# Performance work log

Measured on AMD Instinct MI355X. Metric: run time of the kernel, lower is better.

The kernel has to match this reference:

```python
import jax, jax.numpy as jnp
import numpy as np

N = 100000   # nodes
E = 1600000  # directed edges (avg degree 16)
IN, HID, OUT = 32, 64, 32


def setup_inputs() -> dict:
    key = jax.random.key(0)
    k0, k1, k2, k3 = jax.random.split(key, 4)
    x = jax.random.normal(k0, (N, IN), dtype=jnp.float32)
    edge_index = jax.random.randint(k1, (2, E), 0, N, dtype=jnp.int32)
    W1 = jax.random.normal(k2, (IN, HID), dtype=jnp.float32) * (1.0 / np.sqrt(IN))
    b1 = jnp.zeros((HID,), dtype=jnp.float32)
    W2 = jax.random.normal(k3, (HID, OUT), dtype=jnp.float32) * (1.0 / np.sqrt(HID))
    b2 = jnp.zeros((OUT,), dtype=jnp.float32)
    return {"x": x, "edge_index": edge_index, "W1": W1, "b1": b1, "W2": W2, "b2": b2}


def gcn_conv(x, src, dst, W, b, n):
    # GCNConv: D^{-1/2} (A + I) D^{-1/2} X W + b, deg computed after self-loops
    h = x @ W                                   # [N, d_out]
    ones = jnp.ones_like(dst, dtype=h.dtype)
    deg = jax.ops.segment_sum(ones, dst, num_segments=n)   # >= 1 (self-loops)
    dinv = jax.lax.rsqrt(jnp.maximum(deg, 1.0))
    norm = dinv[src] * dinv[dst]                # [E + N]
    agg = jax.ops.segment_sum(norm[:, None] * h[src], dst, num_segments=n)
    return agg + b


def reference(x, edge_index, W1, b1, W2, b2):
    n = x.shape[0]
    loop = jnp.arange(n, dtype=edge_index.dtype)
    src = jnp.concatenate([edge_index[0], loop])  # add self-loops once
    dst = jnp.concatenate([edge_index[1], loop])
    h = jax.nn.relu(gcn_conv(x, src, dst, W1, b1, n))
    # dropout omitted (eval mode)
    out = gcn_conv(h, src, dst, W2, b2, n)
    return out
```

## Files before the change

kernel.cpp:

```cpp
#include <hip/hip_runtime.h>

#define IN_F  32
#define HID_F 64
#define OUT_F 32

#define BKT_SHIFT 8
#define BKT_NODES 256
#define NBLK      512

__device__ inline unsigned short f2bf(float f) {
    unsigned u = __float_as_uint(f);
    return (unsigned short)((u + 0x7FFF + ((u >> 16) & 1)) >> 16);
}
__device__ inline float bflo(unsigned w) { return __uint_as_float(w << 16); }
__device__ inline float bfhi(unsigned w) { return __uint_as_float(w & 0xFFFF0000u); }

__global__ __launch_bounds__(256) void count_kernel(const int* __restrict__ dst,
                                                    int* __restrict__ cnt, int E, int nb)
{
    __shared__ int hist[1024];
    int tid = threadIdx.x;
    for (int i = tid; i < nb; i += 256) hist[i] = 0;
    __syncthreads();
    for (int e = blockIdx.x * 256 + tid; e < E; e += NBLK * 256)
        atomicAdd(&hist[dst[e] >> BKT_SHIFT], 1);
    __syncthreads();
    for (int i = tid; i < nb; i += 256) cnt[i * NBLK + blockIdx.x] = hist[i];
}

__global__ __launch_bounds__(NBLK) void bsum_kernel(const int* __restrict__ cnt,
                                                    int* __restrict__ bsum)
{
    __shared__ int s[NBLK];
    int tid = threadIdx.x, b = blockIdx.x;
    s[tid] = cnt[b * NBLK + tid];
    __syncthreads();
    for (int off = NBLK / 2; off > 0; off >>= 1) {
        if (tid < off) s[tid] += s[tid + off];
        __syncthreads();
    }
    if (tid == 0) bsum[b] = s[0];
}

__global__ __launch_bounds__(512) void bscan_kernel(int* __restrict__ bsum, int nb,
                                                    int* __restrict__ cellstart, int nc,
                                                    int* __restrict__ rowstart, int n, int E)
{
    __shared__ int s[512];
    int tid = threadIdx.x;
    int my = (tid < nb) ? bsum[tid] : 0;
    s[tid] = my;
    __syncthreads();
    for (int off = 1; off < 512; off <<= 1) {
        int t = (tid >= off) ? s[tid - off] : 0;
        __syncthreads();
        s[tid] += t;
        __syncthreads();
    }
    if (tid < nb) bsum[tid] = s[tid] - my;
    if (tid == 0) { cellstart[nc] = E; rowstart[n] = E; }
}

__global__ __launch_bounds__(NBLK) void cscan_kernel(const int* __restrict__ cnt,
                                                     const int* __restrict__ bsum,
                                                     int* __restrict__ cellstart)
{
    __shared__ int s[NBLK];
    int tid = threadIdx.x, b = blockIdx.x;
    int my = cnt[b * NBLK + tid];
    s[tid] = my;
    __syncthreads();
    for (int off = 1; off < NBLK; off <<= 1) {
        int t = (tid >= off) ? s[tid - off] : 0;
        __syncthreads();
        s[tid] += t;
        __syncthreads();
    }
    cellstart[b * NBLK + tid] = bsum[b] + s[tid] - my;
}

__global__ __launch_bounds__(256) void append_kernel(
    const int* __restrict__ src, const int* __restrict__ dst,
    const int* __restrict__ cellstart, unsigned* __restrict__ pairs, int E, int nb)
{
    __shared__ int cur[1024];
    int tid = threadIdx.x;
    for (int i = tid; i < nb; i += 256) cur[i] = cellstart[i * NBLK + blockIdx.x];
    __syncthreads();
    for (int e = blockIdx.x * 256 + tid; e < E; e += NBLK * 256) {
        int d = dst[e];
        int pos = atomicAdd(&cur[d >> BKT_SHIFT], 1);
        pairs[pos] = ((unsigned)src[e] << BKT_SHIFT) | (unsigned)(d & (BKT_NODES - 1));
    }
}

__global__ __launch_bounds__(256) void place_kernel(
    const int* __restrict__ cellstart, const unsigned* __restrict__ pairs,
    int* __restrict__ srcs, int* __restrict__ rowstart, float* __restrict__ dinv, int n)
{
    __shared__ int hist[BKT_NODES];
    __shared__ int ofs[BKT_NODES];
    int b = blockIdx.x, tid = threadIdx.x;
    int beg = cellstart[b * NBLK], end = cellstart[(b + 1) * NBLK];
    hist[tid] = 0;
    __syncthreads();
    for (int e = beg + tid; e < end; e += 256)
        atomicAdd(&hist[pairs[e] & (BKT_NODES - 1)], 1);
    __syncthreads();
    int my = hist[tid];
    ofs[tid] = my;
    __syncthreads();
    for (int off = 1; off < 256; off <<= 1) {
        int t = (tid >= off) ? ofs[tid - off] : 0;
        __syncthreads();
        ofs[tid] += t;
        __syncthreads();
    }
    int excl = ofs[tid] - my;
    int node = b * BKT_NODES + tid;
    if (node < n) {
        rowstart[node] = beg + excl;
        dinv[node] = rsqrtf((float)(my + 1));
    }
    __syncthreads();
    ofs[tid] = excl;
    __syncthreads();
    for (int e = beg + tid; e < end; e += 256) {
        unsigned p = pairs[e];
        int dl = p & (BKT_NODES - 1);
        int pos = beg + atomicAdd(&ofs[dl], 1);
        srcs[pos] = (int)(p >> BKT_SHIFT);
    }
}

__global__ void xs_kernel(const float* __restrict__ x, const float* __restrict__ dinv,
                          unsigned short* __restrict__ xsb, int n) {
    int t = blockIdx.x * blockDim.x + threadIdx.x;
    if (t < n * (IN_F / 4)) {
        float d = dinv[t >> 3];
        float4 v = ((const float4*)x)[t];
        ushort4 o;
        o.x = f2bf(v.x * d); o.y = f2bf(v.y * d);
        o.z = f2bf(v.z * d); o.w = f2bf(v.w * d);
        ((ushort4*)xsb)[t] = o;
    }
}

__global__ __launch_bounds__(256) void fused1_kernel(
    const int* __restrict__ rowstart, const int* __restrict__ srcs,
    const unsigned* __restrict__ xs2, const float* __restrict__ dinv,
    const float* __restrict__ b1, const float* __restrict__ W1,
    const float* __restrict__ W2, unsigned* __restrict__ hs2p, int n)
{
    __shared__ float W1s[IN_F * HID_F];
    __shared__ float W2s[HID_F * OUT_F];
    __shared__ float grow[16][IN_F + 1];
    __shared__ float hrow[16][HID_F + 1];
    int tid = threadIdx.x;
    for (int t = tid; t < IN_F * HID_F; t += 256) W1s[t] = W1[t];
    for (int t = tid; t < HID_F * OUT_F; t += 256) W2s[t] = W2[t];

    int nl = tid >> 4;
    unsigned q = tid & 15;
    int node = blockIdx.x * 16 + nl;
    bool active = node < n;
    int nodec = active ? node : 0;

    int beg = rowstart[nodec], end = active ? rowstart[nodec + 1] : beg;
    unsigned ws = active ? xs2[((unsigned)nodec << 4) + q] : 0u;
    float a0l = bflo(ws), a0h = bfhi(ws);
    float a1l = 0.f, a1h = 0.f, a2l = 0.f, a2h = 0.f, a3l = 0.f, a3h = 0.f;
    float a4l = 0.f, a4h = 0.f, a5l = 0.f, a5h = 0.f, a6l = 0.f, a6h = 0.f;
    float a7l = 0.f, a7h = 0.f;
    int e = beg;
    for (; e + 8 <= end; e += 8) {
        unsigned o0 = ((unsigned)srcs[e]     << 4) + q, o1 = ((unsigned)srcs[e + 1] << 4) + q;
        unsigned o2 = ((unsigned)srcs[e + 2] << 4) + q, o3 = ((unsigned)srcs[e + 3] << 4) + q;
        unsigned o4 = ((unsigned)srcs[e + 4] << 4) + q, o5 = ((unsigned)srcs[e + 5] << 4) + q;
        unsigned o6 = ((unsigned)srcs[e + 6] << 4) + q, o7 = ((unsigned)srcs[e + 7] << 4) + q;
        unsigned w0 = xs2[o0], w1 = xs2[o1], w2 = xs2[o2], w3 = xs2[o3];
        unsigned w4 = xs2[o4], w5 = xs2[o5], w6 = xs2[o6], w7 = xs2[o7];
        a0l += bflo(w0); a0h += bfhi(w0); a1l += bflo(w1); a1h += bfhi(w1);
        a2l += bflo(w2); a2h += bfhi(w2); a3l += bflo(w3); a3h += bfhi(w3);
        a4l += bflo(w4); a4h += bfhi(w4); a5l += bflo(w5); a5h += bfhi(w5);
        a6l += bflo(w6); a6h += bfhi(w6); a7l += bflo(w7); a7h += bfhi(w7);
    }
    for (; e + 4 <= end; e += 4) {
        unsigned o0 = ((unsigned)srcs[e]     << 4) + q, o1 = ((unsigned)srcs[e + 1] << 4) + q;
        unsigned o2 = ((unsigned)srcs[e + 2] << 4) + q, o3 = ((unsigned)srcs[e + 3] << 4) + q;
        unsigned w0 = xs2[o0], w1 = xs2[o1], w2 = xs2[o2], w3 = xs2[o3];
        a0l += bflo(w0); a0h += bfhi(w0); a1l += bflo(w1); a1h += bfhi(w1);
        a2l += bflo(w2); a2h += bfhi(w2); a3l += bflo(w3); a3h += bfhi(w3);
    }
    for (; e < end; ++e) {
        unsigned w0 = xs2[((unsigned)srcs[e] << 4) + q];
        a0l += bflo(w0); a0h += bfhi(w0);
    }
    float dv = dinv[nodec];
    grow[nl][2 * q]     = dv * (((a0l + a1l) + (a2l + a3l)) + ((a4l + a5l) + (a6l + a7l)));
    grow[nl][2 * q + 1] = dv * (((a0h + a1h) + (a2h + a3h)) + ((a4h + a5h) + (a6h + a7h)));
    __syncthreads();

    float h0 = b1[q], h1 = b1[q + 16], h2 = b1[q + 32], h3 = b1[q + 48];
    #pragma unroll
    for (int k = 0; k < IN_F; ++k) {
        float gk = grow[nl][k];
        h0 += gk * W1s[k * HID_F + q];
        h1 += gk * W1s[k * HID_F + q + 16];
        h2 += gk * W1s[k * HID_F + q + 32];
        h3 += gk * W1s[k * HID_F + q + 48];
    }
    hrow[nl][q]      = fmaxf(h0, 0.f);
    hrow[nl][q + 16] = fmaxf(h1, 0.f);
    hrow[nl][q + 32] = fmaxf(h2, 0.f);
    hrow[nl][q + 48] = fmaxf(h3, 0.f);
    __syncthreads();

    float p0 = 0.f, p1 = 0.f;
    #pragma unroll
    for (int k = 0; k < HID_F; ++k) {
        float hk = hrow[nl][k];
        p0 += hk * W2s[k * OUT_F + 2 * q];
        p1 += hk * W2s[k * OUT_F + 2 * q + 1];
    }
    if (active) {
        unsigned pack = (unsigned)f2bf(dv * p0) | ((unsigned)f2bf(dv * p1) << 16);
        hs2p[((unsigned)node << 4) + q] = pack;
    }
}

__global__ __launch_bounds__(256) void agg2_kernel(
    const int* __restrict__ rowstart, const int* __restrict__ srcs,
    const unsigned* __restrict__ hs2p, const float* __restrict__ dinv,
    const float* __restrict__ b2, float* __restrict__ out, int n)
{
    int t = blockIdx.x * blockDim.x + threadIdx.x;
    int node = t >> 4;
    if (node >= n) return;
    unsigned q = t & 15;
    int beg = rowstart[node], end = rowstart[node + 1];
    unsigned ws = hs2p[((unsigned)node << 4) + q];
    float a0l = bflo(ws), a0h = bfhi(ws);
    float a1l = 0.f, a1h = 0.f, a2l = 0.f, a2h = 0.f, a3l = 0.f, a3h = 0.f;
    float a4l = 0.f, a4h = 0.f, a5l = 0.f, a5h = 0.f, a6l = 0.f, a6h = 0.f;
    float a7l = 0.f, a7h = 0.f;
    int e = beg;
    for (; e + 8 <= end; e += 8) {
        unsigned o0 = ((unsigned)srcs[e]     << 4) + q, o1 = ((unsigned)srcs[e + 1] << 4) + q;
        unsigned o2 = ((unsigned)srcs[e + 2] << 4) + q, o3 = ((unsigned)srcs[e + 3] << 4) + q;
        unsigned o4 = ((unsigned)srcs[e + 4] << 4) + q, o5 = ((unsigned)srcs[e + 5] << 4) + q;
        unsigned o6 = ((unsigned)srcs[e + 6] << 4) + q, o7 = ((unsigned)srcs[e + 7] << 4) + q;
        unsigned w0 = hs2p[o0], w1 = hs2p[o1], w2 = hs2p[o2], w3 = hs2p[o3];
        unsigned w4 = hs2p[o4], w5 = hs2p[o5], w6 = hs2p[o6], w7 = hs2p[o7];
        a0l += bflo(w0); a0h += bfhi(w0); a1l += bflo(w1); a1h += bfhi(w1);
        a2l += bflo(w2); a2h += bfhi(w2); a3l += bflo(w3); a3h += bfhi(w3);
        a4l += bflo(w4); a4h += bfhi(w4); a5l += bflo(w5); a5h += bfhi(w5);
        a6l += bflo(w6); a6h += bfhi(w6); a7l += bflo(w7); a7h += bfhi(w7);
    }
    for (; e + 4 <= end; e += 4) {
        unsigned o0 = ((unsigned)srcs[e]     << 4) + q, o1 = ((unsigned)srcs[e + 1] << 4) + q;
        unsigned o2 = ((unsigned)srcs[e + 2] << 4) + q, o3 = ((unsigned)srcs[e + 3] << 4) + q;
        unsigned w0 = hs2p[o0], w1 = hs2p[o1], w2 = hs2p[o2], w3 = hs2p[o3];
        a0l += bflo(w0); a0h += bfhi(w0); a1l += bflo(w1); a1h += bfhi(w1);
        a2l += bflo(w2); a2h += bfhi(w2); a3l += bflo(w3); a3h += bfhi(w3);
    }
    for (; e < end; ++e) {
        unsigned w0 = hs2p[((unsigned)srcs[e] << 4) + q];
        a0l += bflo(w0); a0h += bfhi(w0);
    }
    float dvv = dinv[node];
    float2 r;
    r.x = dvv * (((a0l + a1l) + (a2l + a3l)) + ((a4l + a5l) + (a6l + a7l))) + b2[2 * q];
    r.y = dvv * (((a0h + a1h) + (a2h + a3h)) + ((a4h + a5h) + (a6h + a7h))) + b2[2 * q + 1];
    ((float2*)out)[((size_t)node << 4) + q] = r;
}

extern "C" void kernel_launch(void* const* d_in, const int* in_sizes, int n_in,
                              void* d_out, int out_size, void* d_ws, size_t ws_size,
                              hipStream_t stream) {
    const float* x  = (const float*)d_in[0];
    const int*   ei = (const int*)  d_in[1];
    const float* W1 = (const float*)d_in[2];
    const float* b1 = (const float*)d_in[3];
    const float* W2 = (const float*)d_in[4];
    const float* b2 = (const float*)d_in[5];
    float* out = (float*)d_out;

    const int n = in_sizes[0] / IN_F;
    const int E = in_sizes[1] / 2;
    const int* src = ei;
    const int* dst = ei + E;

    const int nb = (n + BKT_NODES - 1) >> BKT_SHIFT;
    const int nc = nb * NBLK;

    int* ip = (int*)d_ws;
    int* cnt       = ip;                 ip += nc;
    int* cellstart = ip;                 ip += nc + 1;
    int* bsum      = ip;                 ip += nb + 1;
    int* rowstart  = ip;                 ip += n + 1;
    unsigned* pairs = (unsigned*)ip;     ip += E;
    int* srcs_srt  = ip;                 ip += E;
    float* dinv = (float*)ip;            ip += n;
    unsigned* xs2  = (unsigned*)ip;      ip += (size_t)n * IN_F / 2;
    unsigned* hs2p = (unsigned*)ip;

    count_kernel<<<NBLK, 256, 0, stream>>>(dst, cnt, E, nb);
    bsum_kernel <<<nb, NBLK, 0, stream>>>(cnt, bsum);
    bscan_kernel<<<1, 512, 0, stream>>>(bsum, nb, cellstart, nc, rowstart, n, E);
    cscan_kernel<<<nb, NBLK, 0, stream>>>(cnt, bsum, cellstart);
    append_kernel<<<NBLK, 256, 0, stream>>>(src, dst, cellstart, pairs, E, nb);
    place_kernel<<<nb, 256, 0, stream>>>(cellstart, pairs, srcs_srt, rowstart, dinv, n);

    xs_kernel<<<((size_t)n * 8 + 255) / 256, 256, 0, stream>>>(x, dinv, (unsigned short*)xs2, n);

    fused1_kernel<<<(n + 15) / 16, 256, 0, stream>>>(rowstart, srcs_srt, xs2, dinv, b1, W1, W2, hs2p, n);
    agg2_kernel<<<((size_t)n * 16 + 255) / 256, 256, 0, stream>>>(rowstart, srcs_srt, hs2p, dinv, b2, out, n);
}
```

Measured before the change: 215.5 us.

## Split edge gathers by source-node half to shrink the random-access working set

Edges are bucketed by whether the source lies in the lower or upper half of the node range, which gives two CSR row-start arrays. Each aggregation then runs as two passes, one per source half. The first pass writes float2 partial sums to a buffer and the second adds them in. The aim is to keep each pass's random gather table (about half of 3.2 MB of bf16 features) resident in cache. The cost is two extra kernel launches, extra partial-sum traffic of n×32 floats per layer, a larger scan, and a separate dinv kernel.

Result: slower. 237.0 us (+10.0%).

```diff
diff --git a/kernel.cpp b/kernel.cpp
--- a/kernel.cpp
+++ b/kernel.cpp
@@ -15,15 +15,20 @@
 __device__ inline float bflo(unsigned w) { return __uint_as_float(w << 16); }
 __device__ inline float bfhi(unsigned w) { return __uint_as_float(w & 0xFFFF0000u); }
 
-__global__ __launch_bounds__(256) void count_kernel(const int* __restrict__ dst,
-                                                    int* __restrict__ cnt, int E, int nb)
+__global__ __launch_bounds__(256) void count_kernel(const int* __restrict__ src,
+                                                    const int* __restrict__ dst,
+                                                    int* __restrict__ cnt, int E,
+                                                    int nb0, int half_n)
 {
     __shared__ int hist[1024];
     int tid = threadIdx.x;
+    int nb = 2 * nb0;
     for (int i = tid; i < nb; i += 256) hist[i] = 0;
     __syncthreads();
-    for (int e = blockIdx.x * 256 + tid; e < E; e += NBLK * 256)
-        atomicAdd(&hist[dst[e] >> BKT_SHIFT], 1);
+    for (int e = blockIdx.x * 256 + tid; e < E; e += NBLK * 256) {
+        int cell = ((src[e] >= half_n) ? nb0 : 0) + (dst[e] >> BKT_SHIFT);
+        atomicAdd(&hist[cell], 1);
+    }
     __syncthreads();
     for (int i = tid; i < nb; i += 256) cnt[i * NBLK + blockIdx.x] = hist[i];
 }
@@ -42,23 +47,22 @@
     if (tid == 0) bsum[b] = s[0];
 }
 
-__global__ __launch_bounds__(512) void bscan_kernel(int* __restrict__ bsum, int nb,
-                                                    int* __restrict__ cellstart, int nc,
-                                                    int* __restrict__ rowstart, int n, int E)
-{
-    __shared__ int s[512];
+__global__ __launch_bounds__(1024) void bscan_kernel(int* __restrict__ bsum, int nb,
+                                                     int* __restrict__ cellstart, int nc, int E)
+{
+    __shared__ int s[1024];
     int tid = threadIdx.x;
     int my = (tid < nb) ? bsum[tid] : 0;
     s[tid] = my;
     __syncthreads();
-    for (int off = 1; off < 512; off <<= 1) {
+    for (int off = 1; off < 1024; off <<= 1) {
         int t = (tid >= off) ? s[tid - off] : 0;
         __syncthreads();
         s[tid] += t;
         __syncthreads();
     }
     if (tid < nb) bsum[tid] = s[tid] - my;
-    if (tid == 0) { cellstart[nc] = E; rowstart[n] = E; }
+    if (tid == 0) cellstart[nc] = E;
 }
 
 __global__ __launch_bounds__(NBLK) void cscan_kernel(const int* __restrict__ cnt,
@@ -81,27 +85,34 @@
 
 __global__ __launch_bounds__(256) void append_kernel(
     const int* __restrict__ src, const int* __restrict__ dst,
-    const int* __restrict__ cellstart, unsigned* __restrict__ pairs, int E, int nb)
+    const int* __restrict__ cellstart, unsigned* __restrict__ pairs, int E,
+    int nb0, int half_n)
 {
     __shared__ int cur[1024];
     int tid = threadIdx.x;
+    int nb = 2 * nb0;
     for (int i = tid; i < nb; i += 256) cur[i] = cellstart[i * NBLK + blockIdx.x];
     __syncthreads();
     for (int e = blockIdx.x * 256 + tid; e < E; e += NBLK * 256) {
-        int d = dst[e];
-        int pos = atomicAdd(&cur[d >> BKT_SHIFT], 1);
-        pairs[pos] = ((unsigned)src[e] << BKT_SHIFT) | (unsigned)(d & (BKT_NODES - 1));
+        int s = src[e], d = dst[e];
+        int cell = ((s >= half_n) ? nb0 : 0) + (d >> BKT_SHIFT);
+        int pos = atomicAdd(&cur[cell], 1);
+        pairs[pos] = ((unsigned)s << BKT_SHIFT) | (unsigned)(d & (BKT_NODES - 1));
     }
 }
 
 __global__ __launch_bounds__(256) void place_kernel(
     const int* __restrict__ cellstart, const unsigned* __restrict__ pairs,
-    int* __restrict__ srcs, int* __restrict__ rowstart, float* __restrict__ dinv, int n)
+    int* __restrict__ srcs, int* __restrict__ rs_lo, int* __restrict__ rs_hi,
+    int n, int nb0)
 {
     __shared__ int hist[BKT_NODES];
     __shared__ int ofs[BKT_NODES];
-    int b = blockIdx.x, tid = threadIdx.x;
-    int beg = cellstart[b * NBLK], end = cellstart[(b + 1) * NBLK];
+    int c = blockIdx.x, tid = threadIdx.x;
+    int half = (c >= nb0) ? 1 : 0;
+    int b = c - half * nb0;
+    int* rs = half ? rs_hi : rs_lo;
+    int beg = cellstart[c * NBLK], end = cellstart[(c + 1) * NBLK];
     hist[tid] = 0;
     __syncthreads();
     for (int e = beg + tid; e < end; e += 256)
@@ -118,10 +129,8 @@
     }
     int excl = ofs[tid] - my;
     int node = b * BKT_NODES + tid;
-    if (node < n) {
-        rowstart[node] = beg + excl;
-        dinv[node] = rsqrtf((float)(my + 1));
-    }
+    if (node < n)  rs[node] = beg + excl;
+    if (node == n - 1) rs[n] = beg + excl + my;
     __syncthreads();
     ofs[tid] = excl;
     __syncthreads();
@@ -130,6 +139,16 @@
         int dl = p & (BKT_NODES - 1);
         int pos = beg + atomicAdd(&ofs[dl], 1);
         srcs[pos] = (int)(p >> BKT_SHIFT);
+    }
+}
+
+__global__ void dinv_kernel(const int* __restrict__ rs_lo, const int* __restrict__ rs_hi,
+                            float* __restrict__ dinv, int n)
+{
+    int i = blockIdx.x * blockDim.x + threadIdx.x;
+    if (i < n) {
+        int deg = (rs_lo[i + 1] - rs_lo[i]) + (rs_hi[i + 1] - rs_hi[i]);
+        dinv[i] = rsqrtf((float)(deg + 1));
     }
 }
 
@@ -146,11 +165,55 @@
     }
 }
 
-__global__ __launch_bounds__(256) void fused1_kernel(
-    const int* __restrict__ rowstart, const int* __restrict__ srcs,
-    const unsigned* __restrict__ xs2, const float* __restrict__ dinv,
-    const float* __restrict__ b1, const float* __restrict__ W1,
-    const float* __restrict__ W2, unsigned* __restrict__ hs2p, int n)
+__global__ __launch_bounds__(256) void gather_half_kernel(
+    const int* __restrict__ rs, const int* __restrict__ srcs,
+    const unsigned* __restrict__ tab, float2* __restrict__ acc, int n)
+{
+    int tid = threadIdx.x;
+    int nl = tid >> 4;
+    unsigned q = tid & 15;
+    int node = blockIdx.x * 16 + nl;
+    if (node >= n) return;
+    int beg = rs[node], end = rs[node + 1];
+    float a0l = 0.f, a0h = 0.f, a1l = 0.f, a1h = 0.f, a2l = 0.f, a2h = 0.f;
+    float a3l = 0.f, a3h = 0.f, a4l = 0.f, a4h = 0.f, a5l = 0.f, a5h = 0.f;
+    float a6l = 0.f, a6h = 0.f, a7l = 0.f, a7h = 0.f;
+    int e = beg;
+    for (; e + 8 <= end; e += 8) {
+        unsigned o0 = ((unsigned)srcs[e]     << 4) + q, o1 = ((unsigned)srcs[e + 1] << 4) + q;
+        unsigned o2 = ((unsigned)srcs[e + 2] << 4) + q, o3 = ((unsigned)srcs[e + 3] << 4) + q;
+        unsigned o4 = ((unsigned)srcs[e + 4] << 4) + q, o5 = ((unsigned)srcs[e + 5] << 4) + q;
+        unsigned o6 = ((unsigned)srcs[e + 6] << 4) + q, o7 = ((unsigned)srcs[e + 7] << 4) + q;
+        unsigned w0 = tab[o0], w1 = tab[o1], w2 = tab[o2], w3 = tab[o3];
+        unsigned w4 = tab[o4], w5 = tab[o5], w6 = tab[o6], w7 = tab[o7];
+        a0l += bflo(w0); a0h += bfhi(w0); a1l += bflo(w1); a1h += bfhi(w1);
+        a2l += bflo(w2); a2h += bfhi(w2); a3l += bflo(w3); a3h += bfhi(w3);
+        a4l += bflo(w4); a4h += bfhi(w4); a5l += bflo(w5); a5h += bfhi(w5);
+        a6l += bflo(w6); a6h += bfhi(w6); a7l += bflo(w7); a7h += bfhi(w7);
+    }
+    for (; e + 4 <= end; e += 4) {
+        unsigned o0 = ((unsigned)srcs[e]     << 4) + q, o1 = ((unsigned)srcs[e + 1] << 4) + q;
+        unsigned o2 = ((unsigned)srcs[e + 2] << 4) + q, o3 = ((unsigned)srcs[e + 3] << 4) + q;
+        unsigned w0 = tab[o0], w1 = tab[o1], w2 = tab[o2], w3 = tab[o3];
+        a0l += bflo(w0); a0h += bfhi(w0); a1l += bflo(w1); a1h += bfhi(w1);
+        a2l += bflo(w2); a2h += bfhi(w2); a3l += bflo(w3); a3h += bfhi(w3);
+    }
+    for (; e < end; ++e) {
+        unsigned w0 = tab[((unsigned)srcs[e] << 4) + q];
+        a0l += bflo(w0); a0h += bfhi(w0);
+    }
+    float2 r;
+    r.x = ((a0l + a1l) + (a2l + a3l)) + ((a4l + a5l) + (a6l + a7l));
+    r.y = ((a0h + a1h) + (a2h + a3h)) + ((a4h + a5h) + (a6h + a7h));
+    acc[((unsigned)node << 4) + q] = r;
+}
+
+__global__ __launch_bounds__(256) void fused1b_kernel(
+    const int* __restrict__ rs_hi, const int* __restrict__ srcs,
+    const unsigned* __restrict__ xs2, const float2* __restrict__ acc,
+    const float* __restrict__ dinv, const float* __restrict__ b1,
+    const float* __restrict__ W1, const float* __restrict__ W2,
+    unsigned* __restrict__ hs2p, int n)
 {
     __shared__ float W1s[IN_F * HID_F];
     __shared__ float W2s[HID_F * OUT_F];
@@ -166,12 +229,10 @@
     bool active = node < n;
     int nodec = active ? node : 0;
 
-    int beg = rowstart[nodec], end = active ? rowstart[nodec + 1] : beg;
-    unsigned ws = active ? xs2[((unsigned)nodec << 4) + q] : 0u;
-    float a0l = bflo(ws), a0h = bfhi(ws);
-    float a1l = 0.f, a1h = 0.f, a2l = 0.f, a2h = 0.f, a3l = 0.f, a3h = 0.f;
-    float a4l = 0.f, a4h = 0.f, a5l = 0.f, a5h = 0.f, a6l = 0.f, a6h = 0.f;
-    float a7l = 0.f, a7h = 0.f;
+    int beg = rs_hi[nodec], end = active ? rs_hi[nodec + 1] : beg;
+    float a0l = 0.f, a0h = 0.f, a1l = 0.f, a1h = 0.f, a2l = 0.f, a2h = 0.f;
+    float a3l = 0.f, a3h = 0.f, a4l = 0.f, a4h = 0.f, a5l = 0.f, a5h = 0.f;
+    float a6l = 0.f, a6h = 0.f, a7l = 0.f, a7h = 0.f;
     int e = beg;
     for (; e + 8 <= end; e += 8) {
         unsigned o0 = ((unsigned)srcs[e]     << 4) + q, o1 = ((unsigned)srcs[e + 1] << 4) + q;
@@ -196,9 +257,15 @@
         unsigned w0 = xs2[((unsigned)srcs[e] << 4) + q];
         a0l += bflo(w0); a0h += bfhi(w0);
     }
+    float suml = ((a0l + a1l) + (a2l + a3l)) + ((a4l + a5l) + (a6l + a7l));
+    float sumh = ((a0h + a1h) + (a2h + a3h)) + ((a4h + a5h) + (a6h + a7h));
+    float2 a = acc[((unsigned)nodec << 4) + q];
+    unsigned ws = xs2[((unsigned)nodec << 4) + q];
+    suml += a.x + bflo(ws);
+    sumh += a.y + bfhi(ws);
     float dv = dinv[nodec];
-    grow[nl][2 * q]     = dv * (((a0l + a1l) + (a2l + a3l)) + ((a4l + a5l) + (a6l + a7l)));
-    grow[nl][2 * q + 1] = dv * (((a0h + a1h) + (a2h + a3h)) + ((a4h + a5h) + (a6h + a7h)));
+    grow[nl][2 * q]     = dv * suml;
+    grow[nl][2 * q + 1] = dv * sumh;
     __syncthreads();
 
     float h0 = b1[q], h1 = b1[q + 16], h2 = b1[q + 32], h3 = b1[q + 48];
@@ -229,21 +296,21 @@
     }
 }
 
-__global__ __launch_bounds__(256) void agg2_kernel(
-    const int* __restrict__ rowstart, const int* __restrict__ srcs,
-    const unsigned* __restrict__ hs2p, const float* __restrict__ dinv,
-    const float* __restrict__ b2, float* __restrict__ out, int n)
-{
-    int t = blockIdx.x * blockDim.x + threadIdx.x;
-    int node = t >> 4;
+__global__ __launch_bounds__(256) void agg2hi_kernel(
+    const int* __restrict__ rs_hi, const int* __restrict__ srcs,
+    const unsigned* __restrict__ hs2p, const float2* __restrict__ acc,
+    const float* __restrict__ dinv, const float* __restrict__ b2,
+    float* __restrict__ out, int n)
+{
+    int tid = threadIdx.x;
+    int nl = tid >> 4;
+    unsigned q = tid & 15;
+    int node = blockIdx.x * 16 + nl;
     if (node >= n) return;
-    unsigned q = t & 15;
-    int beg = rowstart[node], end = rowstart[node + 1];
-    unsigned ws = hs2p[((unsigned)node << 4) + q];
-    float a0l = bflo(ws), a0h = bfhi(ws);
-    float a1l = 0.f, a1h = 0.f, a2l = 0.f, a2h = 0.f, a3l = 0.f, a3h = 0.f;
-    float a4l = 0.f, a4h = 0.f, a5l = 0.f, a5h = 0.f, a6l = 0.f, a6h = 0.f;
-    float a7l = 0.f, a7h = 0.f;
+    int beg = rs_hi[node], end = rs_hi[node + 1];
+    float a0l = 0.f, a0h = 0.f, a1l = 0.f, a1h = 0.f, a2l = 0.f, a2h = 0.f;
+    float a3l = 0.f, a3h = 0.f, a4l = 0.f, a4h = 0.f, a5l = 0.f, a5h = 0.f;
+    float a6l = 0.f, a6h = 0.f, a7l = 0.f, a7h = 0.f;
     int e = beg;
     for (; e + 8 <= end; e += 8) {
         unsigned o0 = ((unsigned)srcs[e]     << 4) + q, o1 = ((unsigned)srcs[e + 1] << 4) + q;
@@ -268,10 +335,14 @@
         unsigned w0 = hs2p[((unsigned)srcs[e] << 4) + q];
         a0l += bflo(w0); a0h += bfhi(w0);
     }
+    float2 a = acc[((unsigned)node << 4) + q];
+    unsigned ws = hs2p[((unsigned)node << 4) + q];
+    float suml = ((a0l + a1l) + (a2l + a3l)) + ((a4l + a5l) + (a6l + a7l)) + a.x + bflo(ws);
+    float sumh = ((a0h + a1h) + (a2h + a3h)) + ((a4h + a5h) + (a6h + a7h)) + a.y + bfhi(ws);
     float dvv = dinv[node];
     float2 r;
-    r.x = dvv * (((a0l + a1l) + (a2l + a3l)) + ((a4l + a5l) + (a6l + a7l))) + b2[2 * q];
-    r.y = dvv * (((a0h + a1h) + (a2h + a3h)) + ((a4h + a5h) + (a6h + a7h))) + b2[2 * q + 1];
+    r.x = dvv * suml + b2[2 * q];
+    r.y = dvv * sumh + b2[2 * q + 1];
     ((float2*)out)[((size_t)node << 4) + q] = r;
 }
 
@@ -291,29 +362,36 @@
     const int* src = ei;
     const int* dst = ei + E;
 
-    const int nb = (n + BKT_NODES - 1) >> BKT_SHIFT;
-    const int nc = nb * NBLK;
+    const int half_n = n >> 1;
+    const int nb0 = (n + BKT_NODES - 1) >> BKT_SHIFT;
+    const int nb  = 2 * nb0;
+    const int nc  = nb * NBLK;
 
     int* ip = (int*)d_ws;
     int* cnt       = ip;                 ip += nc;
     int* cellstart = ip;                 ip += nc + 1;
     int* bsum      = ip;                 ip += nb + 1;
-    int* rowstart  = ip;                 ip += n + 1;
+    int* rs_lo     = ip;                 ip += n + 1;
+    int* rs_hi     = ip;                 ip += n + 1;
     unsigned* pairs = (unsigned*)ip;     ip += E;
     int* srcs_srt  = ip;                 ip += E;
     float* dinv = (float*)ip;            ip += n;
     unsigned* xs2  = (unsigned*)ip;      ip += (size_t)n * IN_F / 2;
-    unsigned* hs2p = (unsigned*)ip;
-
-    count_kernel<<<NBLK, 256, 0, stream>>>(dst, cnt, E, nb);
+    unsigned* hs2p = (unsigned*)ip;      ip += (size_t)n * IN_F / 2;
+    float2* acc    = (float2*)ip;
+
+    count_kernel<<<NBLK, 256, 0, stream>>>(src, dst, cnt, E, nb0, half_n);
     bsum_kernel <<<nb, NBLK, 0, stream>>>(cnt, bsum);
-    bscan_kernel<<<1, 512, 0, stream>>>(bsum, nb, cellstart, nc, rowstart, n, E);
+    bscan_kernel<<<1, 1024, 0, stream>>>(bsum, nb, cellstart, nc, E);
     cscan_kernel<<<nb, NBLK, 0, stream>>>(cnt, bsum, cellstart);
-    append_kernel<<<NBLK, 256, 0, stream>>>(src, dst, cellstart, pairs, E, nb);
-    place_kernel<<<nb, 256, 0, stream>>>(cellstart, pairs, srcs_srt, rowstart, dinv, n);
-
+    append_kernel<<<NBLK, 256, 0, stream>>>(src, dst, cellstart, pairs, E, nb0, half_n);
+    place_kernel<<<nb, 256, 0, stream>>>(cellstart, pairs, srcs_srt, rs_lo, rs_hi, n, nb0);
+    dinv_kernel<<<(n + 255) / 256, 256, 0, stream>>>(rs_lo, rs_hi, dinv, n);
     xs_kernel<<<((size_t)n * 8 + 255) / 256, 256, 0, stream>>>(x, dinv, (unsigned short*)xs2, n);
 
-    fused1_kernel<<<(n + 15) / 16, 256, 0, stream>>>(rowstart, srcs_srt, xs2, dinv, b1, W1, W2, hs2p, n);
-    agg2_kernel<<<((size_t)n * 16 + 255) / 256, 256, 0, stream>>>(rowstart, srcs_srt, hs2p, dinv, b2, out, n);
-}
+    const int ngrid = (n + 15) / 16;
+    gather_half_kernel<<<ngrid, 256, 0, stream>>>(rs_lo, srcs_srt, xs2, acc, n);
+    fused1b_kernel<<<ngrid, 256, 0, stream>>>(rs_hi, srcs_srt, xs2, acc, dinv, b1, W1, W2, hs2p, n);
+    gather_half_kernel<<<ngrid, 256, 0, stream>>>(rs_lo, srcs_srt, hs2p, acc, n);
+    agg2hi_kernel<<<ngrid, 256, 0, stream>>>(rs_hi, srcs_srt, hs2p, acc, dinv, b2, out, n);
+}
```

## Fuse bf16 feature scaling into place kernel and widen gathers to 8-byte loads

Applied to the files above, without the earlier changes.

Folds the separate xs_kernel into place_kernel. Each bucket block scales its nodes' features by dinv, kept in shared memory, and writes the packed bf16 table, which removes one launch and one dinv read pass. Both aggregation kernels now have each lane load 8 bytes (four bf16 values) per neighbour, with the two half-groups of 8 lanes working on alternating edges and combined by a shuffle. This halves the number of gather instructions per row. In fused1, the weights are pre-transposed into padded shared layouts for float4/float2 reads, and the intra-kernel barriers are dropped because each node's 16 lanes sit in one wavefront. The risk is relying on wavefront-local LDS ordering in place of the removed barriers, plus some idle lanes in the odd-edge tail and the final output write.

Result: slower. 229.7 us (+6.6%).

```diff
diff --git a/kernel.cpp b/kernel.cpp
--- a/kernel.cpp
+++ b/kernel.cpp
@@ -96,10 +96,13 @@
 
 __global__ __launch_bounds__(256) void place_kernel(
     const int* __restrict__ cellstart, const unsigned* __restrict__ pairs,
-    int* __restrict__ srcs, int* __restrict__ rowstart, float* __restrict__ dinv, int n)
+    const float* __restrict__ x,
+    int* __restrict__ srcs, int* __restrict__ rowstart, float* __restrict__ dinv,
+    unsigned* __restrict__ xs2, int n)
 {
     __shared__ int hist[BKT_NODES];
     __shared__ int ofs[BKT_NODES];
+    __shared__ float sdinv[BKT_NODES];
     int b = blockIdx.x, tid = threadIdx.x;
     int beg = cellstart[b * NBLK], end = cellstart[(b + 1) * NBLK];
     hist[tid] = 0;
@@ -118,9 +121,11 @@
     }
     int excl = ofs[tid] - my;
     int node = b * BKT_NODES + tid;
+    float dv = rsqrtf((float)(my + 1));
+    sdinv[tid] = dv;
     if (node < n) {
         rowstart[node] = beg + excl;
-        dinv[node] = rsqrtf((float)(my + 1));
+        dinv[node] = dv;
     }
     __syncthreads();
     ofs[tid] = excl;
@@ -131,18 +136,18 @@
         int pos = beg + atomicAdd(&ofs[dl], 1);
         srcs[pos] = (int)(p >> BKT_SHIFT);
     }
-}
-
-__global__ void xs_kernel(const float* __restrict__ x, const float* __restrict__ dinv,
-                          unsigned short* __restrict__ xsb, int n) {
-    int t = blockIdx.x * blockDim.x + threadIdx.x;
-    if (t < n * (IN_F / 4)) {
-        float d = dinv[t >> 3];
-        float4 v = ((const float4*)x)[t];
-        ushort4 o;
-        o.x = f2bf(v.x * d); o.y = f2bf(v.y * d);
-        o.z = f2bf(v.z * d); o.w = f2bf(v.w * d);
-        ((ushort4*)xsb)[t] = o;
+    const float4* x4 = (const float4*)x;
+    uint2* xo = (uint2*)xs2;
+    for (int idx = tid; idx < BKT_NODES * 8; idx += 256) {
+        int nloc = idx >> 3, g = idx & 7;
+        int nd = b * BKT_NODES + nloc;
+        if (nd < n) {
+            float d = sdinv[nloc];
+            float4 v = x4[((size_t)nd << 3) + g];
+            unsigned lo = (unsigned)f2bf(v.x * d) | ((unsigned)f2bf(v.y * d) << 16);
+            unsigned hi = (unsigned)f2bf(v.z * d) | ((unsigned)f2bf(v.w * d) << 16);
+            xo[((size_t)nd << 3) + g] = make_uint2(lo, hi);
+        }
     }
 }
 
@@ -152,76 +157,93 @@
     const float* __restrict__ b1, const float* __restrict__ W1,
     const float* __restrict__ W2, unsigned* __restrict__ hs2p, int n)
 {
-    __shared__ float W1s[IN_F * HID_F];
-    __shared__ float W2s[HID_F * OUT_F];
-    __shared__ float grow[16][IN_F + 1];
-    __shared__ float hrow[16][HID_F + 1];
-    int tid = threadIdx.x;
-    for (int t = tid; t < IN_F * HID_F; t += 256) W1s[t] = W1[t];
-    for (int t = tid; t < HID_F * OUT_F; t += 256) W2s[t] = W2[t];
+    __shared__ float W1ps[16 * 132];
+    __shared__ float W2ps[16 * 132];
+    __shared__ float grow[16 * 48];
+    __shared__ float hrow[16 * 80];
+    int tid = threadIdx.x;
+    for (int t = tid; t < 16 * 32; t += 256) {
+        int q = t >> 5, k = t & 31;
+        *(float4*)&W1ps[q * 132 + k * 4] =
+            make_float4(W1[k * HID_F + q],      W1[k * HID_F + q + 16],
+                        W1[k * HID_F + q + 32], W1[k * HID_F + q + 48]);
+    }
+    const float2* W2f2 = (const float2*)W2;
+    for (int t = tid; t < 16 * 64; t += 256) {
+        int q = t >> 6, k = t & 63;
+        *(float2*)&W2ps[q * 132 + k * 2] = W2f2[k * 16 + q];
+    }
+    __syncthreads();
 
     int nl = tid >> 4;
-    unsigned q = tid & 15;
+    int p  = tid & 15;
+    unsigned r = p & 7;
+    int hp = p >> 3;
     int node = blockIdx.x * 16 + nl;
     bool active = node < n;
     int nodec = active ? node : 0;
-
     int beg = rowstart[nodec], end = active ? rowstart[nodec + 1] : beg;
-    unsigned ws = active ? xs2[((unsigned)nodec << 4) + q] : 0u;
-    float a0l = bflo(ws), a0h = bfhi(ws);
-    float a1l = 0.f, a1h = 0.f, a2l = 0.f, a2h = 0.f, a3l = 0.f, a3h = 0.f;
-    float a4l = 0.f, a4h = 0.f, a5l = 0.f, a5h = 0.f, a6l = 0.f, a6h = 0.f;
-    float a7l = 0.f, a7h = 0.f;
+
+    const uint2* tab = (const uint2*)xs2;
+    float a00=0,a01=0,a02=0,a03=0, a10=0,a11=0,a12=0,a13=0;
+    float a20=0,a21=0,a22=0,a23=0, a30=0,a31=0,a32=0,a33=0;
     int e = beg;
     for (; e + 8 <= end; e += 8) {
-        unsigned o0 = ((unsigned)srcs[e]     << 4) + q, o1 = ((unsigned)srcs[e + 1] << 4) + q;
-        unsigned o2 = ((unsigned)srcs[e + 2] << 4) + q, o3 = ((unsigned)srcs[e + 3] << 4) + q;
-        unsigned o4 = ((unsigned)srcs[e + 4] << 4) + q, o5 = ((unsigned)srcs[e + 5] << 4) + q;
-        unsigned o6 = ((unsigned)srcs[e + 6] << 4) + q, o7 = ((unsigned)srcs[e + 7] << 4) + q;
-        unsigned w0 = xs2[o0], w1 = xs2[o1], w2 = xs2[o2], w3 = xs2[o3];
-        unsigned w4 = xs2[o4], w5 = xs2[o5], w6 = xs2[o6], w7 = xs2[o7];
-        a0l += bflo(w0); a0h += bfhi(w0); a1l += bflo(w1); a1h += bfhi(w1);
-        a2l += bflo(w2); a2h += bfhi(w2); a3l += bflo(w3); a3h += bfhi(w3);
-        a4l += bflo(w4); a4h += bfhi(w4); a5l += bflo(w5); a5h += bfhi(w5);
-        a6l += bflo(w6); a6h += bfhi(w6); a7l += bflo(w7); a7h += bfhi(w7);
-    }
-    for (; e + 4 <= end; e += 4) {
-        unsigned o0 = ((unsigned)srcs[e]     << 4) + q, o1 = ((unsigned)srcs[e + 1] << 4) + q;
-        unsigned o2 = ((unsigned)srcs[e + 2] << 4) + q, o3 = ((unsigned)srcs[e + 3] << 4) + q;
-        unsigned w0 = xs2[o0], w1 = xs2[o1], w2 = xs2[o2], w3 = xs2[o3];
-        a0l += bflo(w0); a0h += bfhi(w0); a1l += bflo(w1); a1h += bfhi(w1);
-        a2l += bflo(w2); a2h += bfhi(w2); a3l += bflo(w3); a3h += bfhi(w3);
-    }
-    for (; e < end; ++e) {
-        unsigned w0 = xs2[((unsigned)srcs[e] << 4) + q];
-        a0l += bflo(w0); a0h += bfhi(w0);
-    }
+        int i0 = srcs[e + 0 + hp], i1 = srcs[e + 2 + hp];
+        int i2 = srcs[e + 4 + hp], i3 = srcs[e + 6 + hp];
+        uint2 w0 = tab[((unsigned)i0 << 3) + r];
+        uint2 w1 = tab[((unsigned)i1 << 3) + r];
+        uint2 w2 = tab[((unsigned)i2 << 3) + r];
+        uint2 w3 = tab[((unsigned)i3 << 3) + r];
+        a00 += bflo(w0.x); a01 += bfhi(w0.x); a02 += bflo(w0.y); a03 += bfhi(w0.y);
+        a10 += bflo(w1.x); a11 += bfhi(w1.x); a12 += bflo(w1.y); a13 += bfhi(w1.y);
+        a20 += bflo(w2.x); a21 += bfhi(w2.x); a22 += bflo(w2.y); a23 += bfhi(w2.y);
+        a30 += bflo(w3.x); a31 += bfhi(w3.x); a32 += bflo(w3.y); a33 += bfhi(w3.y);
+    }
+    for (; e + 2 <= end; e += 2) {
+        int i0 = srcs[e + hp];
+        uint2 w0 = tab[((unsigned)i0 << 3) + r];
+        a00 += bflo(w0.x); a01 += bfhi(w0.x); a02 += bflo(w0.y); a03 += bfhi(w0.y);
+    }
+    if (e < end && hp == 0) {
+        int i0 = srcs[e];
+        uint2 w0 = tab[((unsigned)i0 << 3) + r];
+        a00 += bflo(w0.x); a01 += bfhi(w0.x); a02 += bflo(w0.y); a03 += bfhi(w0.y);
+    }
+    if (hp == 0) {
+        uint2 w0 = tab[((unsigned)nodec << 3) + r];
+        a10 += bflo(w0.x); a11 += bfhi(w0.x); a12 += bflo(w0.y); a13 += bfhi(w0.y);
+    }
+    float f0 = (a00 + a10) + (a20 + a30);
+    float f1 = (a01 + a11) + (a21 + a31);
+    float f2 = (a02 + a12) + (a22 + a32);
+    float f3 = (a03 + a13) + (a23 + a33);
+    f0 += __shfl_xor(f0, 8); f1 += __shfl_xor(f1, 8);
+    f2 += __shfl_xor(f2, 8); f3 += __shfl_xor(f3, 8);
     float dv = dinv[nodec];
-    grow[nl][2 * q]     = dv * (((a0l + a1l) + (a2l + a3l)) + ((a4l + a5l) + (a6l + a7l)));
-    grow[nl][2 * q + 1] = dv * (((a0h + a1h) + (a2h + a3h)) + ((a4h + a5h) + (a6h + a7h)));
-    __syncthreads();
-
+    if (hp == 0)
+        *(float4*)&grow[nl * 48 + (int)r * 4] = make_float4(dv*f0, dv*f1, dv*f2, dv*f3);
+
+    int q = p;
     float h0 = b1[q], h1 = b1[q + 16], h2 = b1[q + 32], h3 = b1[q + 48];
+    const float4* w1r = (const float4*)&W1ps[q * 132];
     #pragma unroll
     for (int k = 0; k < IN_F; ++k) {
-        float gk = grow[nl][k];
-        h0 += gk * W1s[k * HID_F + q];
-        h1 += gk * W1s[k * HID_F + q + 16];
-        h2 += gk * W1s[k * HID_F + q + 32];
-        h3 += gk * W1s[k * HID_F + q + 48];
-    }
-    hrow[nl][q]      = fmaxf(h0, 0.f);
-    hrow[nl][q + 16] = fmaxf(h1, 0.f);
-    hrow[nl][q + 32] = fmaxf(h2, 0.f);
-    hrow[nl][q + 48] = fmaxf(h3, 0.f);
-    __syncthreads();
-
+        float gk = grow[nl * 48 + k];
+        float4 w = w1r[k];
+        h0 += gk * w.x; h1 += gk * w.y; h2 += gk * w.z; h3 += gk * w.w;
+    }
+    hrow[nl * 80 + q]      = fmaxf(h0, 0.f);
+    hrow[nl * 80 + q + 16] = fmaxf(h1, 0.f);
+    hrow[nl * 80 + q + 32] = fmaxf(h2, 0.f);
+    hrow[nl * 80 + q + 48] = fmaxf(h3, 0.f);
     float p0 = 0.f, p1 = 0.f;
+    const float2* w2r = (const float2*)&W2ps[q * 132];
     #pragma unroll
     for (int k = 0; k < HID_F; ++k) {
-        float hk = hrow[nl][k];
-        p0 += hk * W2s[k * OUT_F + 2 * q];
-        p1 += hk * W2s[k * OUT_F + 2 * q + 1];
+        float hk = hrow[nl * 80 + k];
+        float2 w = w2r[k];
+        p0 += hk * w.x; p1 += hk * w.y;
     }
     if (active) {
         unsigned pack = (unsigned)f2bf(dv * p0) | ((unsigned)f2bf(dv * p1) << 16);
@@ -234,45 +256,57 @@
     const unsigned* __restrict__ hs2p, const float* __restrict__ dinv,
     const float* __restrict__ b2, float* __restrict__ out, int n)
 {
-    int t = blockIdx.x * blockDim.x + threadIdx.x;
-    int node = t >> 4;
+    int tid = threadIdx.x;
+    int nl = tid >> 4, p = tid & 15;
+    unsigned r = p & 7;
+    int hp = p >> 3;
+    int node = blockIdx.x * 16 + nl;
     if (node >= n) return;
-    unsigned q = t & 15;
     int beg = rowstart[node], end = rowstart[node + 1];
-    unsigned ws = hs2p[((unsigned)node << 4) + q];
-    float a0l = bflo(ws), a0h = bfhi(ws);
-    float a1l = 0.f, a1h = 0.f, a2l = 0.f, a2h = 0.f, a3l = 0.f, a3h = 0.f;
-    float a4l = 0.f, a4h = 0.f, a5l = 0.f, a5h = 0.f, a6l = 0.f, a6h = 0.f;
-    float a7l = 0.f, a7h = 0.f;
+    const uint2* tab = (const uint2*)hs2p;
+    float a00=0,a01=0,a02=0,a03=0, a10=0,a11=0,a12=0,a13=0;
+    float a20=0,a21=0,a22=0,a23=0, a30=0,a31=0,a32=0,a33=0;
     int e = beg;
     for (; e + 8 <= end; e += 8) {
-        unsigned o0 = ((unsigned)srcs[e]     << 4) + q, o1 = ((unsigned)srcs[e + 1] << 4) + q;
-        unsigned o2 = ((unsigned)srcs[e + 2] << 4) + q, o3 = ((unsigned)srcs[e + 3] << 4) + q;
-        unsigned o4 = ((unsigned)srcs[e + 4] << 4) + q, o5 = ((unsigned)srcs[e + 5] << 4) + q;
-        unsigned o6 = ((unsigned)srcs[e + 6] << 4) + q, o7 = ((unsigned)srcs[e + 7] << 4) + q;
-        unsigned w0 = hs2p[o0], w1 = hs2p[o1], w2 = hs2p[o2], w3 = hs2p[o3];
-        unsigned w4 = hs2p[o4], w5 = hs2p[o5], w6 = hs2p[o6], w7 = hs2p[o7];
-        a0l += bflo(w0); a0h += bfhi(w0); a1l += bflo(w1); a1h += bfhi(w1);
-        a2l += bflo(w2); a2h += bfhi(w2); a3l += bflo(w3); a3h += bfhi(w3);
-        a4l += bflo(w4); a4h += bfhi(w4); a5l += bflo(w5); a5h += bfhi(w5);
-        a6l += bflo(w6); a6h += bfhi(w6); a7l += bflo(w7); a7h += bfhi(w7);
-    }
-    for (; e + 4 <= end; e += 4) {
-        unsigned o0 = ((unsigned)srcs[e]     << 4) + q, o1 = ((unsigned)srcs[e + 1] << 4) + q;
-        unsigned o2 = ((unsigned)srcs[e + 2] << 4) + q, o3 = ((unsigned)srcs[e + 3] << 4) + q;
-        unsigned w0 = hs2p[o0], w1 = hs2p[o1], w2 = hs2p[o2], w3 = hs2p[o3];
-        a0l += bflo(w0); a0h += bfhi(w0); a1l += bflo(w1); a1h += bfhi(w1);
-        a2l += bflo(w2); a2h += bfhi(w2); a3l += bflo(w3); a3h += bfhi(w3);
-    }
-    for (; e < end; ++e) {
-        unsigned w0 = hs2p[((unsigned)srcs[e] << 4) + q];
-        a0l += bflo(w0); a0h += bfhi(w0);
-    }
-    float dvv = dinv[node];
-    float2 r;
-    r.x = dvv * (((a0l + a1l) + (a2l + a3l)) + ((a4l + a5l) + (a6l + a7l))) + b2[2 * q];
-    r.y = dvv * (((a0h + a1h) + (a2h + a3h)) + ((a4h + a5h) + (a6h + a7h))) + b2[2 * q + 1];
-    ((float2*)out)[((size_t)node << 4) + q] = r;
+        int i0 = srcs[e + 0 + hp], i1 = srcs[e + 2 + hp];
+        int i2 = srcs[e + 4 + hp], i3 = srcs[e + 6 + hp];
+        uint2 w0 = tab[((unsigned)i0 << 3) + r];
+        uint2 w1 = tab[((unsigned)i1 << 3) + r];
+        uint2 w2 = tab[((unsigned)i2 << 3) + r];
+        uint2 w3 = tab[((unsigned)i3 << 3) + r];
+        a00 += bflo(w0.x); a01 += bfhi(w0.x); a02 += bflo(w0.y); a03 += bfhi(w0.y);
+        a10 += bflo(w1.x); a11 += bfhi(w1.x); a12 += bflo(w1.y); a13 += bfhi(w1.y);
+        a20 += bflo(w2.x); a21 += bfhi(w2.x); a22 += bflo(w2.y); a23 += bfhi(w2.y);
+        a30 += bflo(w3.x); a31 += bfhi(w3.x); a32 += bflo(w3.y); a33 += bfhi(w3.y);
+    }
+    for (; e + 2 <= end; e += 2) {
+        int i0 = srcs[e + hp];
+        uint2 w0 = tab[((unsigned)i0 << 3) + r];
+        a00 += bflo(w0.x); a01 += bfhi(w0.x); a02 += bflo(w0.y); a03 += bfhi(w0.y);
+    }
+    if (e < end && hp == 0) {
+        int i0 = srcs[e];
+        uint2 w0 = tab[((unsigned)i0 << 3) + r];
+        a00 += bflo(w0.x); a01 += bfhi(w0.x); a02 += bflo(w0.y); a03 += bfhi(w0.y);
+    }
+    if (hp == 0) {
+        uint2 w0 = tab[((unsigned)node << 3) + r];
+        a10 += bflo(w0.x); a11 += bfhi(w0.x); a12 += bflo(w0.y); a13 += bfhi(w0.y);
+    }
+    float f0 = (a00 + a10) + (a20 + a30);
+    float f1 = (a01 + a11) + (a21 + a31);
+    float f2 = (a02 + a12) + (a22 + a32);
+    float f3 = (a03 + a13) + (a23 + a33);
+    f0 += __shfl_xor(f0, 8); f1 += __shfl_xor(f1, 8);
+    f2 += __shfl_xor(f2, 8); f3 += __shfl_xor(f3, 8);
+    if (hp == 0) {
+        float dvv = dinv[node];
+        float4 bb = ((const float4*)b2)[r];
+        float4 o;
+        o.x = dvv * f0 + bb.x; o.y = dvv * f1 + bb.y;
+        o.z = dvv * f2 + bb.z; o.w = dvv * f3 + bb.w;
+        ((float4*)out)[((size_t)node << 3) + r] = o;
+    }
 }
 
 extern "C" void kernel_launch(void* const* d_in, const int* in_sizes, int n_in,
@@ -310,10 +344,9 @@
     bscan_kernel<<<1, 512, 0, stream>>>(bsum, nb, cellstart, nc, rowstart, n, E);
     cscan_kernel<<<nb, NBLK, 0, stream>>>(cnt, bsum, cellstart);
     append_kernel<<<NBLK, 256, 0, stream>>>(src, dst, cellstart, pairs, E, nb);
-    place_kernel<<<nb, 256, 0, stream>>>(cellstart, pairs, srcs_srt, rowstart, dinv, n);
-
-    xs_kernel<<<((size_t)n * 8 + 255) / 256, 256, 0, stream>>>(x, dinv, (unsigned short*)xs2, n);
-
-    fused1_kernel<<<(n + 15) / 16, 256, 0, stream>>>(rowstart, srcs_srt, xs2, dinv, b1, W1, W2, hs2p, n);
-    agg2_kernel<<<((size_t)n * 16 + 255) / 256, 256, 0, stream>>>(rowstart, srcs_srt, hs2p, dinv, b2, out, n);
-}
+    place_kernel<<<nb, 256, 0, stream>>>(cellstart, pairs, x, srcs_srt, rowstart, dinv, xs2, n);
+
+    const int ngrid = (n + 15) / 16;
+    fused1_kernel<<<ngrid, 256, 0, stream>>>(rowstart, srcs_srt, xs2, dinv, b1, W1, W2, hs2p, n);
+    agg2_kernel<<<ngrid, 256, 0, stream>>>(rowstart, srcs_srt, hs2p, dinv, b2, out, n);
+}
```
